# Optimization experiments

Measured on AMD Instinct MI355X. Metric: run time of the kernel, lower is better.

## Reference

```python
import jax, jax.numpy as jnp
import numpy as np

NUM_CLASSES = 2
THRESH = 0.5        # overlap_thresh
NEGPOS = 3          # neg:pos ratio
VAR = (0.1, 0.2)    # cfg['variance']
B, P, O = 64, 32768, 50


def point_form(p):
    # center-size [cx,cy,w,h] -> corner [xmin,ymin,xmax,ymax]
    return jnp.concatenate([p[:, :2] - p[:, 2:] * 0.5, p[:, :2] + p[:, 2:] * 0.5], axis=1)


def iou(a, b):
    # a [O,4], b [P,4] corner form -> [O,P]
    lt = jnp.maximum(a[:, None, :2], b[None, :, :2])
    rb = jnp.minimum(a[:, None, 2:], b[None, :, 2:])
    wh = jnp.clip(rb - lt, 0.0, None)
    inter = wh[..., 0] * wh[..., 1]
    area_a = ((a[:, 2] - a[:, 0]) * (a[:, 3] - a[:, 1]))[:, None]
    area_b = ((b[:, 2] - b[:, 0]) * (b[:, 3] - b[:, 1]))[None, :]
    return inter / (area_a + area_b - inter)


def encode(matched, priors_cs):
    g_cxcy = ((matched[:, :2] + matched[:, 2:]) * 0.5 - priors_cs[:, :2]) / (VAR[0] * priors_cs[:, 2:])
    g_wh = jnp.log((matched[:, 2:] - matched[:, :2]) / priors_cs[:, 2:]) / VAR[1]
    return jnp.concatenate([g_cxcy, g_wh], axis=1)


def match_one(truths, labels, priors_cs, priors_pt):
    ovl = iou(truths, priors_pt)                # [O,P]
    best_prior_idx = jnp.argmax(ovl, axis=1)    # [O] best prior per GT
    best_truth_ovl = jnp.max(ovl, axis=0)       # [P]
    best_truth_idx = jnp.argmax(ovl, axis=0)    # [P]
    best_truth_ovl = best_truth_ovl.at[best_prior_idx].set(2.0)
    best_truth_idx = best_truth_idx.at[best_prior_idx].set(jnp.arange(truths.shape[0]))
    matched = truths[best_truth_idx]            # [P,4]
    conf = jnp.where(best_truth_ovl < THRESH, 0, labels[best_truth_idx])
    return encode(matched, priors_cs), conf


def reference(arm_loc, arm_conf, odm_loc, odm_conf, priors, targets):
    loc_data, conf_data = arm_loc, arm_conf    # use_ARM=False -> ARM branch
    num, num_priors = loc_data.shape[0], loc_data.shape[1]
    truths = targets[..., :4]
    labels = (targets[..., 4] >= 0).astype(jnp.int32)   # num_classes == 2 binarization
    priors_pt = point_form(priors)
    loc_t, conf_t = jax.vmap(lambda t, l: match_one(t, l, priors, priors_pt))(truths, labels)
    loc_t = jax.lax.stop_gradient(loc_t)
    conf_t = jax.lax.stop_gradient(conf_t)
    pos = conf_t > 0                             # [B,P]
    # localization: smooth L1, summed over positives
    d = loc_data - loc_t
    ad = jnp.abs(d)
    sl1 = jnp.where(ad < 1.0, 0.5 * d * d, ad - 0.5)
    loss_l = jnp.sum(sl1 * pos[..., None].astype(loc_data.dtype))
    # per-prior conf loss for hard negative mining
    lse = jax.nn.logsumexp(conf_data, axis=-1)   # [B,P]
    picked = jnp.take_along_axis(conf_data, conf_t[..., None], axis=-1)[..., 0]
    lc = lse - picked                            # NLL per prior
    lc_mine = jnp.where(pos, 0.0, lc)            # zero positives before ranking
    order = jnp.argsort(-lc_mine, axis=1)        # descending sort
    rank = jnp.argsort(order, axis=1)            # rank of each prior
    num_pos = jnp.sum(pos, axis=1, keepdims=True)            # [B,1]
    num_neg = jnp.minimum(NEGPOS * num_pos, num_priors - 1)
    neg = rank < num_neg
    sel = (pos | neg).astype(conf_data.dtype)
    loss_c = jnp.sum(lc * sel)
    N = jnp.sum(num_pos).astype(loc_data.dtype)
    return loss_l / N, loss_c / N


def setup_inputs():
    key = jax.random.key(0)
    ks = jax.random.split(key, 8)
    arm_loc = jax.random.normal(ks[0], (B, P, 4), jnp.float32)
    arm_conf = jax.random.normal(ks[1], (B, P, NUM_CLASSES), jnp.float32)
    odm_loc = jax.random.normal(ks[2], (B, P, 4), jnp.float32)
    odm_conf = jax.random.normal(ks[3], (B, P, NUM_CLASSES), jnp.float32)
    # priors in center-size form
    p_cxcy = jax.random.uniform(ks[4], (P, 2), jnp.float32, 0.05, 0.95)
    p_wh = jax.random.uniform(ks[5], (P, 2), jnp.float32, 0.05, 0.5)
    priors = jnp.concatenate([p_cxcy, p_wh], axis=1)
    # GT boxes in corner form with valid extents, labels >= 0
    t_cxcy = jax.random.uniform(ks[6], (B, O, 2), jnp.float32, 0.2, 0.8)
    t_wh = jax.random.uniform(ks[7], (B, O, 2), jnp.float32, 0.05, 0.3)
    boxes = jnp.concatenate([t_cxcy - t_wh * 0.5, t_cxcy + t_wh * 0.5], axis=-1)
    targets = jnp.concatenate([boxes, jnp.ones((B, O, 1), jnp.float32)], axis=-1)
    return {"arm_loc": arm_loc, "arm_conf": arm_conf, "odm_loc": odm_loc,
            "odm_conf": odm_conf, "priors": priors, "targets": targets}
```

## Files before the change

### kernel.cpp

```cpp
#include <hip/hip_runtime.h>
#include <cstdint>

#pragma clang fp contract(off)

#define BB 64
#define PP 32768
#define OO 50
#define THRESH_F 0.5f
#define VAR0 0.1f
#define VAR1 0.2f
#define NEGPOS_I 3
#define SS 32
#define T1 4
#define NB0 2048
#define NB12 1024
#define NCELL 1024

typedef unsigned long long u64;

__device__ __forceinline__ unsigned mpart4(unsigned x) {
    x = (x | (x << 2)) & 0x33u;
    x = (x | (x << 1)) & 0x55u;
    return x;
}
__device__ __forceinline__ int cell_of(float4 pr) {
    int xb = (int)(pr.x * 16.0f); xb = xb < 0 ? 0 : (xb > 15 ? 15 : xb);
    int yb = (int)(pr.y * 16.0f); yb = yb < 0 ? 0 : (yb > 15 ? 15 : yb);
    float s = fmaxf(pr.z, pr.w);
    int wc = s < 0.275f ? 0 : (s < 0.368f ? 1 : (s < 0.44f ? 2 : 3));
    return wc * 256 + (int)(mpart4((unsigned)xb) | (mpart4((unsigned)yb) << 1));
}

__global__ void k_zero(float4* __restrict__ dst, int n4) {
    int i = blockIdx.x * blockDim.x + threadIdx.x;
    if (i < n4) dst[i] = make_float4(0.f, 0.f, 0.f, 0.f);
}

__global__ void k_phist(const float4* __restrict__ pri, int* __restrict__ cnt) {
    int p = blockIdx.x * 1024 + threadIdx.x * 4;
    for (int j = 0; j < 4; ++j)
        atomicAdd(&cnt[cell_of(pri[p + j])], 1);
}

__global__ void __launch_bounds__(256)
k_pss(const float4* __restrict__ pri, const int* __restrict__ cnt,
      int* __restrict__ cursor, int* __restrict__ perm, int* __restrict__ iperm) {
    __shared__ int sc[256];
    __shared__ int sbase[NCELL];
    int tid = threadIdx.x;
    int a[4]; int s = 0;
    for (int i = 0; i < 4; ++i) { a[i] = cnt[tid * 4 + i]; s += a[i]; }
    sc[tid] = s; __syncthreads();
    for (int off = 1; off < 256; off <<= 1) {
        int v = (tid >= off) ? sc[tid - off] : 0;
        __syncthreads(); sc[tid] += v; __syncthreads();
    }
    int excl = sc[tid] - s;
    for (int i = 0; i < 4; ++i) { sbase[tid * 4 + i] = excl; excl += a[i]; }
    __syncthreads();
    int p = blockIdx.x * 1024 + tid * 4;
    for (int j = 0; j < 4; ++j) {
        int c = cell_of(pri[p + j]);
        int pos = sbase[c] + atomicAdd(&cursor[c], 1);
        perm[pos] = p + j;
        iperm[p + j] = pos;
    }
}

#define DPP_MAX(x, ctrl, rmask)                                              \
    {                                                                        \
        int _o = __float_as_int(x);                                          \
        x = fmaxf(x, __int_as_float(__builtin_amdgcn_update_dpp(             \
                _o, _o, (ctrl), (rmask), 0xf, false)));                      \
    }
#define DPP_MINF(x, ctrl, rmask)                                             \
    {                                                                        \
        int _o = __float_as_int(x);                                          \
        x = fminf(x, __int_as_float(__builtin_amdgcn_update_dpp(             \
                _o, _o, (ctrl), (rmask), 0xf, false)));                      \
    }
#define DPP_MINI(x, ctrl, rmask)                                             \
    {                                                                        \
        int _o = (x);                                                        \
        int _s = __builtin_amdgcn_update_dpp(_o, _o, (ctrl), (rmask), 0xf, false); \
        x = (_s < x) ? _s : x;                                               \
    }
#define WAVE_MAXF(x) { DPP_MAX(x,0x111,0xf); DPP_MAX(x,0x112,0xf); DPP_MAX(x,0x114,0xf); \
                       DPP_MAX(x,0x118,0xf); DPP_MAX(x,0x142,0xa); DPP_MAX(x,0x143,0xc); }
#define WAVE_MINF(x) { DPP_MINF(x,0x111,0xf); DPP_MINF(x,0x112,0xf); DPP_MINF(x,0x114,0xf); \
                       DPP_MINF(x,0x118,0xf); DPP_MINF(x,0x142,0xa); DPP_MINF(x,0x143,0xc); }
#define WAVE_MINI(x) { DPP_MINI(x,0x111,0xf); DPP_MINI(x,0x112,0xf); DPP_MINI(x,0x114,0xf); \
                       DPP_MINI(x,0x118,0xf); DPP_MINI(x,0x142,0xa); DPP_MINI(x,0x143,0xc); }

__device__ __forceinline__ float sl1enc(const float* __restrict__ tb,
                                        float4 pr, float4 ld) {
    float gx = ((tb[0] + tb[2]) * 0.5f - pr.x) / (VAR0 * pr.z);
    float gy = ((tb[1] + tb[3]) * 0.5f - pr.y) / (VAR0 * pr.w);
    float gw = logf((tb[2] - tb[0]) / pr.z) / VAR1;
    float gh = logf((tb[3] - tb[1]) / pr.w) / VAR1;
    float g[4] = {gx, gy, gw, gh};
    float l[4] = {ld.x, ld.y, ld.z, ld.w};
    float s = 0.f;
    for (int q = 0; q < 4; ++q) {
        float d = l[q] - g[q];
        float ad = fabsf(d);
        s += (ad < 1.0f) ? 0.5f * d * d : ad - 0.5f;
    }
    return s;
}

__global__ void __launch_bounds__(256, 8)
k_ml(const float* __restrict__ priors, const int* __restrict__ perm,
     const float* __restrict__ targets,
     const float* __restrict__ arm_loc, const float* __restrict__ arm_conf,
     float* __restrict__ lcmP, unsigned char* __restrict__ bpiP,
     u64* __restrict__ bpm,
     float* __restrict__ pll, float* __restrict__ pplc, int* __restrict__ pnp,
     int* __restrict__ Hc0, float* __restrict__ Hs0) {
    __shared__ float4 trP[OO];
    __shared__ float2 trQ[OO];
    __shared__ int   hc[NB0];
    __shared__ float hs[NB0];
    int b = (blockIdx.x % 8) * 8 + (blockIdx.y % 8);
    int s = (blockIdx.x / 8) + 4 * (blockIdx.y / 8);
    int tid = threadIdx.x;
    if (tid < OO) {
        const float* tb = &targets[(size_t)(b * OO + tid) * 5];
        float x0 = tb[0], y0 = tb[1], x1 = tb[2], y1 = tb[3];
        trP[tid] = make_float4(x0, y0, x1, y1);
        trQ[tid] = make_float2((x1 - x0) * (y1 - y0), tb[4]);
    }
    for (int i = tid; i < NB0; i += 256) { hc[i] = 0; hs[i] = 0.f; }
    __syncthreads();

    int p0 = s * (256 * T1) + tid * T1;
    int4 o4 = ((const int4*)perm)[p0 >> 2];
    int o_[T1] = {o4.x, o4.y, o4.z, o4.w};
    int omin = min(min(o_[0], o_[1]), min(o_[2], o_[3]));
    float bx0[T1], by0[T1], bx1[T1], by1[T1], aB[T1];
#pragma unroll
    for (int j = 0; j < T1; ++j) {
        float4 pr = ((const float4*)priors)[o_[j]];
        bx0[j] = pr.x - pr.z * 0.5f; by0[j] = pr.y - pr.w * 0.5f;
        bx1[j] = pr.x + pr.z * 0.5f; by1[j] = pr.y + pr.w * 0.5f;
        aB[j] = (bx1[j] - bx0[j]) * (by1[j] - by0[j]);
    }
    float lx0 = fminf(fminf(bx0[0], bx0[1]), fminf(bx0[2], bx0[3]));
    float ly0 = fminf(fminf(by0[0], by0[1]), fminf(by0[2], by0[3]));
    float lx1 = fmaxf(fmaxf(bx1[0], bx1[1]), fmaxf(bx1[2], bx1[3]));
    float ly1 = fmaxf(fmaxf(by1[0], by1[1]), fmaxf(by1[2], by1[3]));
    WAVE_MINF(lx0); WAVE_MINF(ly0); WAVE_MAXF(lx1); WAVE_MAXF(ly1);
    float wx0 = __int_as_float(__builtin_amdgcn_readlane(__float_as_int(lx0), 63));
    float wy0 = __int_as_float(__builtin_amdgcn_readlane(__float_as_int(ly0), 63));
    float wx1 = __int_as_float(__builtin_amdgcn_readlane(__float_as_int(lx1), 63));
    float wy1 = __int_as_float(__builtin_amdgcn_readlane(__float_as_int(ly1), 63));

    float rbv[T1]; int rbi[T1];
#pragma unroll
    for (int j = 0; j < T1; ++j) { rbv[j] = 0.0f; rbi[j] = 0; }

    for (int t = 0; t < OO; ++t) {
        float4 tP = trP[t];
        if (!(tP.z > wx0 && tP.x < wx1 && tP.w > wy0 && tP.y < wy1)) continue;
        float aA = trQ[t].x;
        float I[T1];
#pragma unroll
        for (int j = 0; j < T1; ++j) {
            float ltx = fmaxf(tP.x, bx0[j]), lty = fmaxf(tP.y, by0[j]);
            float rbx = fminf(tP.z, bx1[j]), rby = fminf(tP.w, by1[j]);
            float wx = fmaxf(rbx - ltx, 0.f), wy = fmaxf(rby - lty, 0.f);
            I[j] = wx * wy;
        }
        bool anyl = (I[0] > 0.f) | (I[1] > 0.f) | (I[2] > 0.f) | (I[3] > 0.f);
        if (__any(anyl)) {
            float cbv = 0.0f; int cbo = omin;
#pragma unroll
            for (int j = 0; j < T1; ++j) {
                float v = I[j] / (aA + aB[j] - I[j]);
                if (v > rbv[j]) { rbv[j] = v; rbi[j] = t; }
                if (v > cbv || (v == cbv && o_[j] < cbo)) { cbv = v; cbo = o_[j]; }
            }
            float x = cbv;
            WAVE_MAXF(x);
            float mvf = __int_as_float(__builtin_amdgcn_readlane(__float_as_int(x), 63));
            if (mvf > 0.0f) {
                int key = (cbv == mvf) ? cbo : 0x7FFFFFFF;
                WAVE_MINI(key);
                int morig = __builtin_amdgcn_readlane(key, 63);
                if ((tid & 63) == 0) {
                    u64 pk = ((u64)__float_as_uint(mvf) << 32) | (unsigned)(PP - morig);
                    atomicMax(&bpm[b * OO + t], pk);
                }
            }
        }
    }

    size_t bbase = (size_t)b * PP;
    float ll = 0.0f, plc = 0.0f; int np = 0;
    float outv[4]; unsigned pbyte = 0;
#pragma unroll
    for (int c = 0; c < T1; ++c) {
        int o = o_[c]; size_t bo = bbase + o;
        int ti = rbi[c]; float ov = rbv[c];
        float2 cf = ((const float2*)arm_conf)[bo];
        float c0 = cf.x, c1 = cf.y;
        float m = fmaxf(c0, c1);
        float lse = logf(expf(c0 - m) + expf(c1 - m)) + m;
        bool pos = (ov >= THRESH_F) && (trQ[ti].y >= 0.0f);
        float lc = lse - (pos ? c1 : c0);
        outv[c] = pos ? 0.0f : lc;
        pbyte |= (unsigned)((pos ? 0x80u : 0u) | (unsigned)ti) << (8 * c);
        unsigned u = __float_as_uint(outv[c]);
        atomicAdd(&hc[u >> 20], 1);
        atomicAdd(&hs[u >> 20], outv[c]);
        if (pos) {
            np++; plc += lc;
            float4 pr = ((const float4*)priors)[o];
            float4 ld = ((const float4*)arm_loc)[bo];
            const float4 tv = trP[ti];
            float tb4[4] = {tv.x, tv.y, tv.z, tv.w};
            ll += sl1enc(tb4, pr, ld);
        }
    }
    size_t bq = bbase + p0;
    ((float4*)lcmP)[bq >> 2] = make_float4(outv[0], outv[1], outv[2], outv[3]);
    ((unsigned*)bpiP)[bq >> 2] = pbyte;

    __syncthreads();
    for (int i = tid; i < NB0; i += 256) {
        int cv = hc[i];
        if (cv) {
            atomicAdd(&Hc0[b * NB0 + i], cv);
            atomicAdd(&Hs0[b * NB0 + i], hs[i]);
        }
    }
    __syncthreads();
    float* s1 = (float*)hc;
    int*   s3 = hc + 256;
    float* s2 = hs;
    s1[tid] = ll; s2[tid] = plc; s3[tid] = np;
    __syncthreads();
    for (int st = 128; st > 0; st >>= 1) {
        if (tid < st) { s1[tid] += s1[tid+st]; s2[tid] += s2[tid+st]; s3[tid] += s3[tid+st]; }
        __syncthreads();
    }
    if (tid == 0) {
        pll[s * BB + b] = s1[0];
        pplc[s * BB + b] = s2[0];
        pnp[s * BB + b] = s3[0];
    }
}

__global__ void __launch_bounds__(256)
k_tail(const u64* __restrict__ bpm, const float* __restrict__ targets,
       const float* __restrict__ arm_loc, const float* __restrict__ arm_conf,
       const float* __restrict__ priors, const int* __restrict__ iperm,
       float* __restrict__ lcmP, const unsigned char* __restrict__ bpiP,
       const float* __restrict__ pll, const float* __restrict__ pplc,
       const int* __restrict__ pnp,
       int* __restrict__ Hc0, float* __restrict__ Hs0,
       float* __restrict__ gacc, int* __restrict__ gcnt,
       float* __restrict__ out) {
    __shared__ int hc[NB12]; __shared__ float hs[NB12];
    __shared__ int sc[256]; __shared__ float sf[256];
    __shared__ int s_chunk, s_r; __shared__ float s_S; __shared__ unsigned s_pref;
    __shared__ float s_llb, s_plcb; __shared__ int s_npb;
    int b = blockIdx.x, tid = threadIdx.x;
    size_t bbase = (size_t)b * PP;

    if (tid < 64) {
        int j = tid;
        int p = -1;
        if (j < OO) {
            unsigned lo = (unsigned)(bpm[b * OO + j] & 0xFFFFFFFFull);
            p = lo ? (PP - (int)lo) : 0;
        }
        bool w = (j < OO);
        for (int jj = 1; jj < OO; ++jj) {
            int pj = __shfl(p, jj, 64);
            if (jj > j && pj == p) w = false;
        }
        float dll = 0.f, dplc = 0.f; int dnp = 0;
        if (w) {
            int pos = iperm[p];
            size_t bq = bbase + pos;
            size_t bo = bbase + p;
            unsigned char ob = bpiP[bq];
            bool old_pos = (ob & 0x80u) != 0;
            int old_ti = ob & 63;
            float2 cf = ((const float2*)arm_conf)[bo];
            float c0 = cf.x, c1 = cf.y;
            float m = fmaxf(c0, c1);
            float lse = logf(expf(c0 - m) + expf(c1 - m)) + m;
            const float* tbj = &targets[(size_t)(b * OO + j) * 5];
            bool new_pos = (tbj[4] >= 0.0f);
            float old_lcm = lcmP[bq];
            float new_lcm = new_pos ? 0.0f : (lse - c0);
            unsigned uo = __float_as_uint(old_lcm), un = __float_as_uint(new_lcm);
            if (uo != un) {
                atomicAdd(&Hc0[b * NB0 + (uo >> 20)], -1);
                atomicAdd(&Hs0[b * NB0 + (uo >> 20)], -old_lcm);
                atomicAdd(&Hc0[b * NB0 + (un >> 20)], 1);
                atomicAdd(&Hs0[b * NB0 + (un >> 20)], new_lcm);
                atomicExch(&lcmP[bq], new_lcm);
            }
            float4 pr = ((const float4*)priors)[p];
            float4 ld = ((const float4*)arm_loc)[bo];
            if (old_pos) {
                dnp -= 1; dplc -= (lse - c1);
                dll -= sl1enc(&targets[(size_t)(b * OO + old_ti) * 5], pr, ld);
            }
            if (new_pos) {
                dnp += 1; dplc += (lse - c1);
                dll += sl1enc(tbj, pr, ld);
            }
        }
        float myll = (j < SS) ? pll[j * BB + b] : 0.f;
        float mypl = (j < SS) ? pplc[j * BB + b] : 0.f;
        int   mynp = (j < SS) ? pnp[j * BB + b] : 0;
        dll += myll; dplc += mypl; dnp += mynp;
        for (int st = 32; st >= 1; st >>= 1) {
            dll += __shfl_down(dll, st, 64);
            dplc += __shfl_down(dplc, st, 64);
            dnp += __shfl_down(dnp, st, 64);
        }
        if (j == 0) { s_llb = dll; s_plcb = dplc; s_npb = dnp; }
    }
    __threadfence();
    __syncthreads();

    {
        const int* hcg = Hc0 + b * NB0; const float* hsg = Hs0 + b * NB0;
        int c = 0; float f = 0.f; int base = tid * 8;
        for (int i = 0; i < 8; ++i) { c += hcg[base + i]; f += hsg[base + i]; }
        sc[tid] = c; sf[tid] = f;
        if (tid == 0) {
            int k = NEGPOS_I * s_npb; if (k > PP - 1) k = PP - 1;
            s_r = k; s_S = 0.f;
        }
        __syncthreads();
        for (int off = 1; off < 256; off <<= 1) {
            int cv = (tid + off < 256) ? sc[tid + off] : 0;
            float fv = (tid + off < 256) ? sf[tid + off] : 0.f;
            __syncthreads(); sc[tid] += cv; sf[tid] += fv; __syncthreads();
        }
        int r = s_r;
        int nxt = (tid == 255) ? 0 : sc[tid + 1];
        if (sc[tid] >= r && nxt < r) s_chunk = tid;
        __syncthreads();
        if (tid == 0) {
            int ch = s_chunk;
            int r2 = r - ((ch == 255) ? 0 : sc[ch + 1]);
            float S2 = s_S + ((ch == 255) ? 0.f : sf[ch + 1]);
            int binSel = ch * 8;
            for (int i = 7; i >= 0; --i) {
                int bin = ch * 8 + i; int cbn = hcg[bin];
                if (r2 <= cbn) { binSel = bin; break; }
                r2 -= cbn; S2 += hsg[bin];
            }
            s_pref = (unsigned)binSel; s_r = r2; s_S = S2;
        }
        __syncthreads();
    }
    {
        for (int i = tid; i < NB12; i += 256) { hc[i] = 0; hs[i] = 0.f; }
        __syncthreads();
        unsigned pref = s_pref;
        const float4* v4 = (const float4*)(lcmP + bbase);
        for (int it = 0; it < 32; ++it) {
            float4 x = v4[it * 256 + tid];
            float xs[4] = {x.x, x.y, x.z, x.w};
            for (int c2 = 0; c2 < 4; ++c2) {
                unsigned u = __float_as_uint(xs[c2]);
                if ((u >> 20) == pref) {
                    atomicAdd(&hc[(u >> 10) & 1023u], 1);
                    atomicAdd(&hs[(u >> 10) & 1023u], xs[c2]);
                }
            }
        }
        __syncthreads();
        int c = 0; float f = 0.f; int base = tid * 4;
        for (int i = 0; i < 4; ++i) { c += hc[base + i]; f += hs[base + i]; }
        sc[tid] = c; sf[tid] = f; __syncthreads();
        for (int off = 1; off < 256; off <<= 1) {
            int cv = (tid + off < 256) ? sc[tid + off] : 0;
            float fv = (tid + off < 256) ? sf[tid + off] : 0.f;
            __syncthreads(); sc[tid] += cv; sf[tid] += fv; __syncthreads();
        }
        int r = s_r;
        int nxt = (tid == 255) ? 0 : sc[tid + 1];
        if (sc[tid] >= r && nxt < r) s_chunk = tid;
        __syncthreads();
        if (tid == 0) {
            int ch = s_chunk;
            int r2 = r - ((ch == 255) ? 0 : sc[ch + 1]);
            float S2 = s_S + ((ch == 255) ? 0.f : sf[ch + 1]);
            int binSel = ch * 4;
            for (int i = 3; i >= 0; --i) {
                int bin = ch * 4 + i; int cbn = hc[bin];
                if (r2 <= cbn) { binSel = bin; break; }
                r2 -= cbn; S2 += hs[bin];
            }
            s_pref = (s_pref << 10) | (unsigned)binSel; s_r = r2; s_S = S2;
        }
        __syncthreads();
    }
    {
        for (int i = tid; i < NB12; i += 256) { hc[i] = 0; hs[i] = 0.f; }
        __syncthreads();
        unsigned pref = s_pref;
        const float4* v4 = (const float4*)(lcmP + bbase);
        for (int it = 0; it < 32; ++it) {
            float4 x = v4[it * 256 + tid];
            float xs[4] = {x.x, x.y, x.z, x.w};
            for (int c2 = 0; c2 < 4; ++c2) {
                unsigned u = __float_as_uint(xs[c2]);
                if ((u >> 10) == pref) {
                    atomicAdd(&hc[u & 1023u], 1);
                    atomicAdd(&hs[u & 1023u], xs[c2]);
                }
            }
        }
        __syncthreads();
        int c = 0; float f = 0.f; int base = tid * 4;
        for (int i = 0; i < 4; ++i) { c += hc[base + i]; f += hs[base + i]; }
        sc[tid] = c; sf[tid] = f; __syncthreads();
        for (int off = 1; off < 256; off <<= 1) {
            int cv = (tid + off < 256) ? sc[tid + off] : 0;
            float fv = (tid + off < 256) ? sf[tid + off] : 0.f;
            __syncthreads(); sc[tid] += cv; sf[tid] += fv; __syncthreads();
        }
        int r = s_r;
        int nxt = (tid == 255) ? 0 : sc[tid + 1];
        if (sc[tid] >= r && nxt < r) s_chunk = tid;
        __syncthreads();
        if (tid == 0) {
            int ch = s_chunk;
            int r2 = r - ((ch == 255) ? 0 : sc[ch + 1]);
            float S2 = s_S + ((ch == 255) ? 0.f : sf[ch + 1]);
            int binSel = ch * 4;
            for (int i = 3; i >= 0; --i) {
                int bin = ch * 4 + i; int cbn = hc[bin];
                if (r2 <= cbn) { binSel = bin; break; }
                r2 -= cbn; S2 += hs[bin];
            }
            unsigned tb = (s_pref << 10) | (unsigned)binSel;
            float tval = __uint_as_float(tb);
            float ccb = s_plcb + S2 + (float)r2 * tval;
            float llb = s_llb; int npb = s_npb;
            float oll = atomicAdd(&gacc[0], llb);
            float occ = atomicAdd(&gacc[1], ccb);
            int onp = atomicAdd(&gcnt[0], npb);
            __threadfence();
            int tk = atomicAdd(&gcnt[1], 1);
            if (tk == BB - 1) {
                float N = (float)(onp + npb);
                out[0] = (oll + llb) / N;
                out[1] = (occ + ccb) / N;
            }
        }
    }
}

extern "C" void kernel_launch(void* const* d_in, const int* in_sizes, int n_in,
                              void* d_out, int out_size, void* d_ws, size_t ws_size,
                              hipStream_t stream) {
    const float* arm_loc  = (const float*)d_in[0];
    const float* arm_conf = (const float*)d_in[1];
    const float* priors   = (const float*)d_in[4];
    const float* targets  = (const float*)d_in[5];
    float* out = (float*)d_out;

    char* w = (char*)d_ws;
    float* lcmP = (float*)w;  w += sizeof(float) * (size_t)BB * PP;
    unsigned char* bpiP = (unsigned char*)w; w += (size_t)BB * PP;
    char* zbase = w;
    int*   Hc0 = (int*)w;    w += sizeof(int)   * BB * NB0;
    float* Hs0 = (float*)w;  w += sizeof(float) * BB * NB0;
    u64*   bpm = (u64*)w;    w += sizeof(u64)   * BB * OO;
    int*   cellCnt = (int*)w; w += sizeof(int) * NCELL;
    int*   cursor  = (int*)w; w += sizeof(int) * NCELL;
    float* gacc = (float*)w;  w += sizeof(float) * 2;
    int*   gcnt = (int*)w;    w += sizeof(int) * 2;
    size_t zbytes = (size_t)(w - zbase);
    int*   perm  = (int*)w;  w += sizeof(int) * PP;
    int*   iperm = (int*)w;  w += sizeof(int) * PP;
    float* pll  = (float*)w; w += sizeof(float) * BB * SS;
    float* pplc = (float*)w; w += sizeof(float) * BB * SS;
    int*   pnp  = (int*)w;   w += sizeof(int)   * BB * SS;

    int n4 = (int)(zbytes / 16);
    k_zero<<<(n4 + 255) / 256, 256, 0, stream>>>((float4*)zbase, n4);
    k_phist<<<PP / 1024, 256, 0, stream>>>((const float4*)priors, cellCnt);
    k_pss<<<PP / 1024, 256, 0, stream>>>((const float4*)priors, cellCnt, cursor, perm, iperm);
    k_ml<<<dim3(SS, BB), 256, 0, stream>>>(priors, perm, targets, arm_loc, arm_conf,
                                           lcmP, bpiP, bpm, pll, pplc, pnp, Hc0, Hs0);
    k_tail<<<BB, 256, 0, stream>>>(bpm, targets, arm_loc, arm_conf, priors, iperm,
                                   lcmP, bpiP, pll, pplc, pnp, Hc0, Hs0, gacc, gcnt, out);
}
```

Baseline: 274.8 us.

## Move first-level histogram from k_ml into selection kernel and split tail kernels

Removes the per-block shared-memory histogram build and the global atomic histogram merge from the main match kernel, and rebuilds the coarse histogram inside a new selection kernel by rereading lcmP. The tail work is split into three kernels: k_fix applies the forced-match corrections, k_sel does the top-k threshold selection, and k_final does a deterministic reduction in place of global atomics. The wave-wide min-index DPP reduction is replaced by a ballot plus a readlane loop. In exchange, the per-image loss array gets one extra full pass and two more kernel launches are added.

```diff
diff --git a/kernel.cpp b/kernel.cpp
--- a/kernel.cpp
+++ b/kernel.cpp
@@ -79,18 +79,10 @@
         x = fminf(x, __int_as_float(__builtin_amdgcn_update_dpp(             \
                 _o, _o, (ctrl), (rmask), 0xf, false)));                      \
     }
-#define DPP_MINI(x, ctrl, rmask)                                             \
-    {                                                                        \
-        int _o = (x);                                                        \
-        int _s = __builtin_amdgcn_update_dpp(_o, _o, (ctrl), (rmask), 0xf, false); \
-        x = (_s < x) ? _s : x;                                               \
-    }
 #define WAVE_MAXF(x) { DPP_MAX(x,0x111,0xf); DPP_MAX(x,0x112,0xf); DPP_MAX(x,0x114,0xf); \
                        DPP_MAX(x,0x118,0xf); DPP_MAX(x,0x142,0xa); DPP_MAX(x,0x143,0xc); }
 #define WAVE_MINF(x) { DPP_MINF(x,0x111,0xf); DPP_MINF(x,0x112,0xf); DPP_MINF(x,0x114,0xf); \
                        DPP_MINF(x,0x118,0xf); DPP_MINF(x,0x142,0xa); DPP_MINF(x,0x143,0xc); }
-#define WAVE_MINI(x) { DPP_MINI(x,0x111,0xf); DPP_MINI(x,0x112,0xf); DPP_MINI(x,0x114,0xf); \
-                       DPP_MINI(x,0x118,0xf); DPP_MINI(x,0x142,0xa); DPP_MINI(x,0x143,0xc); }
 
 __device__ __forceinline__ float sl1enc(const float* __restrict__ tb,
                                         float4 pr, float4 ld) {
@@ -115,12 +107,10 @@
      const float* __restrict__ arm_loc, const float* __restrict__ arm_conf,
      float* __restrict__ lcmP, unsigned char* __restrict__ bpiP,
      u64* __restrict__ bpm,
-     float* __restrict__ pll, float* __restrict__ pplc, int* __restrict__ pnp,
-     int* __restrict__ Hc0, float* __restrict__ Hs0) {
+     float* __restrict__ pll, float* __restrict__ pplc, int* __restrict__ pnp) {
     __shared__ float4 trP[OO];
     __shared__ float2 trQ[OO];
-    __shared__ int   hc[NB0];
-    __shared__ float hs[NB0];
+    __shared__ float s1[256]; __shared__ float s2[256]; __shared__ int s3[256];
     int b = (blockIdx.x % 8) * 8 + (blockIdx.y % 8);
     int s = (blockIdx.x / 8) + 4 * (blockIdx.y / 8);
     int tid = threadIdx.x;
@@ -130,7 +120,6 @@
         trP[tid] = make_float4(x0, y0, x1, y1);
         trQ[tid] = make_float2((x1 - x0) * (y1 - y0), tb[4]);
     }
-    for (int i = tid; i < NB0; i += 256) { hc[i] = 0; hs[i] = 0.f; }
     __syncthreads();
 
     int p0 = s * (256 * T1) + tid * T1;
@@ -184,9 +173,16 @@
             WAVE_MAXF(x);
             float mvf = __int_as_float(__builtin_amdgcn_readlane(__float_as_int(x), 63));
             if (mvf > 0.0f) {
-                int key = (cbv == mvf) ? cbo : 0x7FFFFFFF;
-                WAVE_MINI(key);
-                int morig = __builtin_amdgcn_readlane(key, 63);
+                u64 msk = __ballot(cbv == mvf);
+                int ln = (int)__ffsll((long long)msk) - 1;
+                int morig = __builtin_amdgcn_readlane(cbo, ln);
+                u64 rest = msk & (msk - 1);
+                while (rest) {
+                    int l2 = (int)__ffsll((long long)rest) - 1;
+                    int o2 = __builtin_amdgcn_readlane(cbo, l2);
+                    morig = min(morig, o2);
+                    rest &= rest - 1;
+                }
                 if ((tid & 63) == 0) {
                     u64 pk = ((u64)__float_as_uint(mvf) << 32) | (unsigned)(PP - morig);
                     atomicMax(&bpm[b * OO + t], pk);
@@ -210,9 +206,6 @@
         float lc = lse - (pos ? c1 : c0);
         outv[c] = pos ? 0.0f : lc;
         pbyte |= (unsigned)((pos ? 0x80u : 0u) | (unsigned)ti) << (8 * c);
-        unsigned u = __float_as_uint(outv[c]);
-        atomicAdd(&hc[u >> 20], 1);
-        atomicAdd(&hs[u >> 20], outv[c]);
         if (pos) {
             np++; plc += lc;
             float4 pr = ((const float4*)priors)[o];
@@ -226,18 +219,6 @@
     ((float4*)lcmP)[bq >> 2] = make_float4(outv[0], outv[1], outv[2], outv[3]);
     ((unsigned*)bpiP)[bq >> 2] = pbyte;
 
-    __syncthreads();
-    for (int i = tid; i < NB0; i += 256) {
-        int cv = hc[i];
-        if (cv) {
-            atomicAdd(&Hc0[b * NB0 + i], cv);
-            atomicAdd(&Hs0[b * NB0 + i], hs[i]);
-        }
-    }
-    __syncthreads();
-    float* s1 = (float*)hc;
-    int*   s3 = hc + 256;
-    float* s2 = hs;
     s1[tid] = ll; s2[tid] = plc; s3[tid] = np;
     __syncthreads();
     for (int st = 128; st > 0; st >>= 1) {
@@ -251,91 +232,92 @@
     }
 }
 
+__global__ void k_fix(const u64* __restrict__ bpm, const float* __restrict__ targets,
+                      const float* __restrict__ arm_loc, const float* __restrict__ arm_conf,
+                      const float* __restrict__ priors, const int* __restrict__ iperm,
+                      const unsigned char* __restrict__ bpiP, float* __restrict__ lcmP,
+                      float* __restrict__ pll, float* __restrict__ pplc,
+                      int* __restrict__ pnp, int* __restrict__ npb) {
+    int b = blockIdx.x, j = threadIdx.x;
+    int p = -1;
+    if (j < OO) {
+        unsigned lo = (unsigned)(bpm[b * OO + j] & 0xFFFFFFFFull);
+        p = lo ? (PP - (int)lo) : 0;
+    }
+    bool w = (j < OO);
+    for (int jj = 1; jj < OO; ++jj) {
+        int pj = __shfl(p, jj, 64);
+        if (jj > j && pj == p) w = false;
+    }
+    float dll = 0.f, dplc = 0.f; int dnp = 0;
+    if (w) {
+        int pos_ = iperm[p];
+        size_t bq = (size_t)b * PP + pos_;
+        size_t bo = (size_t)b * PP + p;
+        unsigned char ob = bpiP[bq];
+        bool old_pos = (ob & 0x80u) != 0;
+        int old_ti = ob & 63;
+        float2 cf = ((const float2*)arm_conf)[bo];
+        float c0 = cf.x, c1 = cf.y;
+        float m = fmaxf(c0, c1);
+        float lse = logf(expf(c0 - m) + expf(c1 - m)) + m;
+        const float* tbj = &targets[(size_t)(b * OO + j) * 5];
+        bool new_pos = (tbj[4] >= 0.0f);
+        float new_lcm = new_pos ? 0.0f : (lse - c0);
+        lcmP[bq] = new_lcm;
+        float4 pr = ((const float4*)priors)[p];
+        float4 ld = ((const float4*)arm_loc)[bo];
+        if (old_pos) {
+            dnp -= 1; dplc -= (lse - c1);
+            dll -= sl1enc(&targets[(size_t)(b * OO + old_ti) * 5], pr, ld);
+        }
+        if (new_pos) {
+            dnp += 1; dplc += (lse - c1);
+            dll += sl1enc(tbj, pr, ld);
+        }
+    }
+    int myp = (j < SS) ? pnp[j * BB + b] : 0;
+    for (int st = 32; st >= 1; st >>= 1) {
+        dll += __shfl_down(dll, st, 64);
+        dplc += __shfl_down(dplc, st, 64);
+        dnp += __shfl_down(dnp, st, 64);
+        myp += __shfl_down(myp, st, 64);
+    }
+    if (j == 0) {
+        pll[b] += dll;
+        pplc[b] += dplc;
+        pnp[b] += dnp;
+        npb[b] = myp + dnp;
+    }
+}
+
 __global__ void __launch_bounds__(256)
-k_tail(const u64* __restrict__ bpm, const float* __restrict__ targets,
-       const float* __restrict__ arm_loc, const float* __restrict__ arm_conf,
-       const float* __restrict__ priors, const int* __restrict__ iperm,
-       float* __restrict__ lcmP, const unsigned char* __restrict__ bpiP,
-       const float* __restrict__ pll, const float* __restrict__ pplc,
-       const int* __restrict__ pnp,
-       int* __restrict__ Hc0, float* __restrict__ Hs0,
-       float* __restrict__ gacc, int* __restrict__ gcnt,
-       float* __restrict__ out) {
-    __shared__ int hc[NB12]; __shared__ float hs[NB12];
+k_sel(const float* __restrict__ lcmP, const int* __restrict__ npb,
+      float* __restrict__ ssum, int* __restrict__ srem, unsigned* __restrict__ stb) {
+    __shared__ int hc[NB0]; __shared__ float hs[NB0];
     __shared__ int sc[256]; __shared__ float sf[256];
     __shared__ int s_chunk, s_r; __shared__ float s_S; __shared__ unsigned s_pref;
-    __shared__ float s_llb, s_plcb; __shared__ int s_npb;
     int b = blockIdx.x, tid = threadIdx.x;
-    size_t bbase = (size_t)b * PP;
-
-    if (tid < 64) {
-        int j = tid;
-        int p = -1;
-        if (j < OO) {
-            unsigned lo = (unsigned)(bpm[b * OO + j] & 0xFFFFFFFFull);
-            p = lo ? (PP - (int)lo) : 0;
-        }
-        bool w = (j < OO);
-        for (int jj = 1; jj < OO; ++jj) {
-            int pj = __shfl(p, jj, 64);
-            if (jj > j && pj == p) w = false;
-        }
-        float dll = 0.f, dplc = 0.f; int dnp = 0;
-        if (w) {
-            int pos = iperm[p];
-            size_t bq = bbase + pos;
-            size_t bo = bbase + p;
-            unsigned char ob = bpiP[bq];
-            bool old_pos = (ob & 0x80u) != 0;
-            int old_ti = ob & 63;
-            float2 cf = ((const float2*)arm_conf)[bo];
-            float c0 = cf.x, c1 = cf.y;
-            float m = fmaxf(c0, c1);
-            float lse = logf(expf(c0 - m) + expf(c1 - m)) + m;
-            const float* tbj = &targets[(size_t)(b * OO + j) * 5];
-            bool new_pos = (tbj[4] >= 0.0f);
-            float old_lcm = lcmP[bq];
-            float new_lcm = new_pos ? 0.0f : (lse - c0);
-            unsigned uo = __float_as_uint(old_lcm), un = __float_as_uint(new_lcm);
-            if (uo != un) {
-                atomicAdd(&Hc0[b * NB0 + (uo >> 20)], -1);
-                atomicAdd(&Hs0[b * NB0 + (uo >> 20)], -old_lcm);
-                atomicAdd(&Hc0[b * NB0 + (un >> 20)], 1);
-                atomicAdd(&Hs0[b * NB0 + (un >> 20)], new_lcm);
-                atomicExch(&lcmP[bq], new_lcm);
-            }
-            float4 pr = ((const float4*)priors)[p];
-            float4 ld = ((const float4*)arm_loc)[bo];
-            if (old_pos) {
-                dnp -= 1; dplc -= (lse - c1);
-                dll -= sl1enc(&targets[(size_t)(b * OO + old_ti) * 5], pr, ld);
-            }
-            if (new_pos) {
-                dnp += 1; dplc += (lse - c1);
-                dll += sl1enc(tbj, pr, ld);
-            }
-        }
-        float myll = (j < SS) ? pll[j * BB + b] : 0.f;
-        float mypl = (j < SS) ? pplc[j * BB + b] : 0.f;
-        int   mynp = (j < SS) ? pnp[j * BB + b] : 0;
-        dll += myll; dplc += mypl; dnp += mynp;
-        for (int st = 32; st >= 1; st >>= 1) {
-            dll += __shfl_down(dll, st, 64);
-            dplc += __shfl_down(dplc, st, 64);
-            dnp += __shfl_down(dnp, st, 64);
-        }
-        if (j == 0) { s_llb = dll; s_plcb = dplc; s_npb = dnp; }
-    }
-    __threadfence();
-    __syncthreads();
+    const float4* v4 = (const float4*)(lcmP + (size_t)b * PP);
 
     {
-        const int* hcg = Hc0 + b * NB0; const float* hsg = Hs0 + b * NB0;
+        for (int i = tid; i < NB0; i += 256) { hc[i] = 0; hs[i] = 0.f; }
+        __syncthreads();
+        for (int it = 0; it < 32; ++it) {
+            float4 x = v4[it * 256 + tid];
+            float xs[4] = {x.x, x.y, x.z, x.w};
+            for (int c2 = 0; c2 < 4; ++c2) {
+                unsigned u = __float_as_uint(xs[c2]);
+                atomicAdd(&hc[u >> 20], 1);
+                atomicAdd(&hs[u >> 20], xs[c2]);
+            }
+        }
+        __syncthreads();
         int c = 0; float f = 0.f; int base = tid * 8;
-        for (int i = 0; i < 8; ++i) { c += hcg[base + i]; f += hsg[base + i]; }
+        for (int i = 0; i < 8; ++i) { c += hc[base + i]; f += hs[base + i]; }
         sc[tid] = c; sf[tid] = f;
         if (tid == 0) {
-            int k = NEGPOS_I * s_npb; if (k > PP - 1) k = PP - 1;
+            int k = NEGPOS_I * npb[b]; if (k > PP - 1) k = PP - 1;
             s_r = k; s_S = 0.f;
         }
         __syncthreads();
@@ -354,9 +336,9 @@
             float S2 = s_S + ((ch == 255) ? 0.f : sf[ch + 1]);
             int binSel = ch * 8;
             for (int i = 7; i >= 0; --i) {
-                int bin = ch * 8 + i; int cbn = hcg[bin];
+                int bin = ch * 8 + i; int cbn = hc[bin];
                 if (r2 <= cbn) { binSel = bin; break; }
-                r2 -= cbn; S2 += hsg[bin];
+                r2 -= cbn; S2 += hs[bin];
             }
             s_pref = (unsigned)binSel; s_r = r2; s_S = S2;
         }
@@ -366,7 +348,6 @@
         for (int i = tid; i < NB12; i += 256) { hc[i] = 0; hs[i] = 0.f; }
         __syncthreads();
         unsigned pref = s_pref;
-        const float4* v4 = (const float4*)(lcmP + bbase);
         for (int it = 0; it < 32; ++it) {
             float4 x = v4[it * 256 + tid];
             float xs[4] = {x.x, x.y, x.z, x.w};
@@ -409,7 +390,6 @@
         for (int i = tid; i < NB12; i += 256) { hc[i] = 0; hs[i] = 0.f; }
         __syncthreads();
         unsigned pref = s_pref;
-        const float4* v4 = (const float4*)(lcmP + bbase);
         for (int it = 0; it < 32; ++it) {
             float4 x = v4[it * 256 + tid];
             float xs[4] = {x.x, x.y, x.z, x.w};
@@ -444,21 +424,34 @@
                 if (r2 <= cbn) { binSel = bin; break; }
                 r2 -= cbn; S2 += hs[bin];
             }
-            unsigned tb = (s_pref << 10) | (unsigned)binSel;
-            float tval = __uint_as_float(tb);
-            float ccb = s_plcb + S2 + (float)r2 * tval;
-            float llb = s_llb; int npb = s_npb;
-            float oll = atomicAdd(&gacc[0], llb);
-            float occ = atomicAdd(&gacc[1], ccb);
-            int onp = atomicAdd(&gcnt[0], npb);
-            __threadfence();
-            int tk = atomicAdd(&gcnt[1], 1);
-            if (tk == BB - 1) {
-                float N = (float)(onp + npb);
-                out[0] = (oll + llb) / N;
-                out[1] = (occ + ccb) / N;
-            }
-        }
+            stb[b] = (s_pref << 10) | (unsigned)binSel;
+            srem[b] = r2; ssum[b] = S2;
+        }
+    }
+}
+
+__global__ void k_final(const float* __restrict__ pll, const float* __restrict__ pplc,
+                        const int* __restrict__ pnp, const float* __restrict__ ssum,
+                        const int* __restrict__ srem, const unsigned* __restrict__ stb,
+                        float* __restrict__ out) {
+    int b = threadIdx.x;
+    float ll = 0.f, plc = 0.f; int np = 0;
+    for (int s = 0; s < SS; ++s) {
+        ll += pll[s * BB + b];
+        plc += pplc[s * BB + b];
+        np += pnp[s * BB + b];
+    }
+    float tval = __uint_as_float(stb[b]);
+    float cc = plc + ssum[b] + (float)srem[b] * tval;
+    for (int s = 32; s > 0; s >>= 1) {
+        ll += __shfl_down(ll, s);
+        cc += __shfl_down(cc, s);
+        np += __shfl_down(np, s);
+    }
+    if (b == 0) {
+        float N = (float)np;
+        out[0] = ll / N;
+        out[1] = cc / N;
     }
 }
 
@@ -475,26 +468,28 @@
     float* lcmP = (float*)w;  w += sizeof(float) * (size_t)BB * PP;
     unsigned char* bpiP = (unsigned char*)w; w += (size_t)BB * PP;
     char* zbase = w;
-    int*   Hc0 = (int*)w;    w += sizeof(int)   * BB * NB0;
-    float* Hs0 = (float*)w;  w += sizeof(float) * BB * NB0;
-    u64*   bpm = (u64*)w;    w += sizeof(u64)   * BB * OO;
     int*   cellCnt = (int*)w; w += sizeof(int) * NCELL;
     int*   cursor  = (int*)w; w += sizeof(int) * NCELL;
-    float* gacc = (float*)w;  w += sizeof(float) * 2;
-    int*   gcnt = (int*)w;    w += sizeof(int) * 2;
+    u64*   bpm = (u64*)w;    w += sizeof(u64)   * BB * OO;
     size_t zbytes = (size_t)(w - zbase);
     int*   perm  = (int*)w;  w += sizeof(int) * PP;
     int*   iperm = (int*)w;  w += sizeof(int) * PP;
     float* pll  = (float*)w; w += sizeof(float) * BB * SS;
     float* pplc = (float*)w; w += sizeof(float) * BB * SS;
     int*   pnp  = (int*)w;   w += sizeof(int)   * BB * SS;
+    int*   npb  = (int*)w;   w += sizeof(int)   * BB;
+    int*      srem = (int*)w;      w += sizeof(int) * BB;
+    float*    ssum = (float*)w;    w += sizeof(float) * BB;
+    unsigned* stb  = (unsigned*)w; w += sizeof(unsigned) * BB;
 
     int n4 = (int)(zbytes / 16);
     k_zero<<<(n4 + 255) / 256, 256, 0, stream>>>((float4*)zbase, n4);
     k_phist<<<PP / 1024, 256, 0, stream>>>((const float4*)priors, cellCnt);
     k_pss<<<PP / 1024, 256, 0, stream>>>((const float4*)priors, cellCnt, cursor, perm, iperm);
     k_ml<<<dim3(SS, BB), 256, 0, stream>>>(priors, perm, targets, arm_loc, arm_conf,
-                                           lcmP, bpiP, bpm, pll, pplc, pnp, Hc0, Hs0);
-    k_tail<<<BB, 256, 0, stream>>>(bpm, targets, arm_loc, arm_conf, priors, iperm,
-                                   lcmP, bpiP, pll, pplc, pnp, Hc0, Hs0, gacc, gcnt, out);
-}
+                                           lcmP, bpiP, bpm, pll, pplc, pnp);
+    k_fix<<<BB, 64, 0, stream>>>(bpm, targets, arm_loc, arm_conf, priors, iperm,
+                                 bpiP, lcmP, pll, pplc, pnp, npb);
+    k_sel<<<BB, 256, 0, stream>>>(lcmP, npb, ssum, srem, stb);
+    k_final<<<1, 64, 0, stream>>>(pll, pplc, pnp, ssum, srem, stb, out);
+}
```

Measured after the change: 304.5 us. 1.11x slower.
